# Kernel tuning notes

Measured on AMD Instinct MI355X. Metric: run time of the kernel, lower is better.

## Reference

```python
import jax, jax.numpy as jnp
import numpy as np

B, S = 512, 256          # batch, seq_len
C, H = 8, 16             # num_cells, expert hidden size
M = 20                   # memory_size (hard-coded in module)
NT = C * H               # num_trajectories = 128
ENC_IN = M * (NT + 1)    # 20*129 = 2580, memory_encode input dim
A_H = 16                 # agent LSTM hidden


def setup_inputs() -> dict:
    key = jax.random.key(0)
    ks = jax.random.split(key, 20)
    r = lambda i, shape: 0.1 * jax.random.normal(ks[i], shape, dtype=jnp.float32)
    return {
        "x": jax.random.normal(ks[0], (B, S, 1), dtype=jnp.float32),
        "pred0": jax.random.uniform(ks[1], (B, 1), dtype=jnp.float32),
        "gate0": jax.nn.softmax(jax.random.uniform(ks[2], (B, C), dtype=jnp.float32), axis=1),
        # experts: C parallel LSTM cells (input 1, hidden H) + per-cell scalar head
        "W_ih": r(3, (C, 4 * H, 1)), "W_hh": r(4, (C, 4 * H, H)),
        "b_ih": r(5, (C, 4 * H)), "b_hh": r(6, (C, 4 * H)),
        "W_o": r(7, (C, H)), "b_o": r(8, (C,)),
        # memory_encode: Linear(2580,64) ReLU Linear(64,16) ReLU
        "W1": r(9, (64, ENC_IN)), "b1": r(10, (64,)),
        "W2": r(11, (16, 64)), "b2": r(12, (16,)),
        # gate_linear: Linear(16, C) + softmax
        "Wg": r(13, (C, 16)), "bg": r(14, (C,)),
        # agent: 2 stacked LSTM cells (16 -> 16)
        "Wa_ih": r(15, (2, 4 * A_H, A_H)), "Wa_hh": r(16, (2, 4 * A_H, A_H)),
        "ba_ih": r(17, (2, 4 * A_H)), "ba_hh": r(18, (2, 4 * A_H)),
    }


def _cell(z, c):
    # PyTorch LSTMCell gate order: i, f, g, o
    i, f, g, o = jnp.split(z, 4, axis=-1)
    c2 = jax.nn.sigmoid(f) * c + jax.nn.sigmoid(i) * jnp.tanh(g)
    return jax.nn.sigmoid(o) * jnp.tanh(c2), c2


def reference(x, pred0, gate0, W_ih, W_hh, b_ih, b_hh, W_o, b_o,
              W1, b1, W2, b2, Wg, bg, Wa_ih, Wa_hh, ba_ih, ba_hh):
    mem0 = jnp.zeros((B, M, NT + 1), jnp.float32).at[:, :, -1].set(0.5)
    eh0 = jnp.zeros((B, H), jnp.float32)   # combined expert h (shared across cells)
    a0 = jnp.zeros((2, B, A_H), jnp.float32)

    def step(carry, x_t):
        mem, eh, ec, pred, gate_state, ah, ac = carry
        error = x_t - pred                                        # [B,1]
        # experts: C LSTM cells, all reading the shared combined state
        z = (jnp.einsum('bf,cgf->bcg', x_t, W_ih)
             + jnp.einsum('bh,cgh->bcg', eh, W_hh)
             + b_ih + b_hh)                                       # [B,C,4H]
        nh, nc = _cell(z, ec[:, None, :])                          # [B,C,H]
        o = jnp.einsum('bch,ch->bc', nh, W_o) + b_o               # [B,C]
        # memory_step: matmul(mstep, mem) shifts rows down by 1, row 0 <- w
        w = jnp.concatenate([nh.reshape(B, -1), error], axis=1)   # [B,NT+1]
        mem = jnp.concatenate([w[:, None, :], mem[:, :-1, :]], axis=1)
        # memory_encode MLP
        e1 = jax.nn.relu(mem.reshape(B, -1) @ W1.T + b1)
        ai = jax.nn.relu(e1 @ W2.T + b2)                           # [B,16]
        # agent: 2 stacked LSTM cells
        ah_l, ac_l, inp_l = [], [], ai
        for l in range(2):
            zl = inp_l @ Wa_ih[l].T + ba_ih[l] + ah[l] @ Wa_hh[l].T + ba_hh[l]
            hl, cl = _cell(zl, ac[l])
            ah_l.append(hl); ac_l.append(cl)
            inp_l = hl
        ah2, ac2 = jnp.stack(ah_l), jnp.stack(ac_l)
        gate = jax.nn.softmax(inp_l @ Wg.T + bg, axis=1)           # [B,C]
        # theta = clip(2.5 * mean|mem[:, :10, -1]|, 0, 1)  (relu(t)-relu(t-1))
        theta = jnp.clip(jnp.mean(jnp.abs(mem[:, :10, -1]), axis=1) * 2.5, 0.0, 1.0)[:, None]
        gate = gate * theta + gate_state * (1.0 - theta)
        eh2 = jnp.einsum('bc,bch->bh', gate, nh)                   # bmm(gate, h)
        ec2 = jnp.einsum('bc,bch->bh', gate, nc)
        pred2 = jnp.einsum('bc,bc->b', gate, o)[:, None]           # [B,1]
        return (mem, eh2, ec2, pred2, gate, ah2, ac2), pred2

    xs = jnp.swapaxes(x, 0, 1)  # [S,B,1]
    _, preds = jax.lax.scan(step, (mem0, eh0, eh0, pred0, gate0, a0, a0), xs)
    return jnp.swapaxes(preds, 0, 1)  # [B,S,1]
```

## Files before the change

kernel.cpp:

```cpp
#include <hip/hip_runtime.h>
#include <math.h>

#define S_LEN 256
#define NCELL 8
#define HID 16
#define MEM 20
#define NB 4
#define NTHR 512
#define RSTR 2592
#define RP 80

typedef _Float16 v8h __attribute__((ext_vector_type(8)));
typedef _Float16 v4h __attribute__((ext_vector_type(4)));
typedef float v4f __attribute__((ext_vector_type(4)));

__device__ __forceinline__ float sigm(float v) { return 1.0f / (1.0f + __expf(-v)); }
__device__ __forceinline__ float tanh_f(float v) { return 1.0f - 2.0f / (__expf(2.0f * v) + 1.0f); }
__device__ __forceinline__ float dot4(float4 a, float4 b) {
    return fmaf(a.x, b.x, fmaf(a.y, b.y, fmaf(a.z, b.z, a.w * b.w)));
}
__device__ __forceinline__ v4f mfma16(v8h a, v8h b, v4f c) {
    return __builtin_amdgcn_mfma_f32_16x16x32_f16(a, b, c, 0, 0, 0);
}

#define RING(b, s, k) ringH[(b) * RSTR + (s) * 128 + (k)]

__global__ __launch_bounds__(256)
void prep_w(const float* __restrict__ W1, const float* __restrict__ W_hh,
            const float* __restrict__ W_ih, const float* __restrict__ b_ih,
            const float* __restrict__ b_hh, _Float16* __restrict__ W1F,
            _Float16* __restrict__ WAF) {
    int idx = blockIdx.x * 256 + threadIdx.x;
    if (idx < 163840) {
        int e = idx & 7, lane = (idx >> 3) & 63, jt = (idx >> 9) & 3, t = idx >> 11;
        int m = t >> 2, kc = t & 3;
        int j = jt * 16 + (lane & 15);
        int k = kc * 32 + (lane >> 4) * 8 + e;
        W1F[idx] = (_Float16)W1[j * 2580 + m * 129 + k];
    } else if (idx < 163840 + 16384) {
        int d = idx - 163840;
        int e = d & 7, lane = (d >> 3) & 63, gate = (d >> 9) & 3, c = d >> 11;
        int m = lane & 15, k = (lane >> 4) * 8 + e;
        int row = c * 64 + gate * 16 + m;
        float v = 0.f;
        if (k < 16) v = W_hh[row * 16 + k];
        else if (k == 16) v = W_ih[row];
        else if (k == 17) v = b_ih[row] + b_hh[row];
        WAF[d] = (_Float16)v;
    }
}

#define E1P(BB, V) { \
    V = b1_l[lane] \
      + red[par][1][BB][lane] + red[par][2][BB][lane] + red[par][3][BB][lane] \
      + red[par][4][BB][lane] + red[par][5][BB][lane] + red[par][6][BB][lane] \
      + red[par][7][BB][lane]; }

#define E1F(BB, V) { \
    V += errdotS[BB][lane] \
       + red0[0][BB][lane] + red0[1][BB][lane] + red0[2][BB][lane] + red0[3][BB][lane]; \
    e1S[BB][lane] = fmaxf(V, 0.f); }

__global__ __attribute__((amdgpu_flat_work_group_size(NTHR, NTHR)))
void mmoe_kernel(const float* __restrict__ x, const float* __restrict__ pred0,
                 const float* __restrict__ gate0,
                 const float* __restrict__ W_ih, const float* __restrict__ W_hh,
                 const float* __restrict__ b_ih, const float* __restrict__ b_hh,
                 const float* __restrict__ W_o, const float* __restrict__ b_o,
                 const float* __restrict__ W1, const float* __restrict__ b1,
                 const float* __restrict__ W2, const float* __restrict__ b2,
                 const float* __restrict__ Wg, const float* __restrict__ bg,
                 const float* __restrict__ Wa_ih, const float* __restrict__ Wa_hh,
                 const float* __restrict__ ba_ih, const float* __restrict__ ba_hh,
                 const _Float16* __restrict__ W1F, const _Float16* __restrict__ WAF,
                 float* __restrict__ out)
{
    __shared__ __align__(16) _Float16 ringH[NB * RSTR];
    __shared__ __align__(16) _Float16 ehH[NB][40];
    __shared__ float errS[NB][MEM];
    __shared__ __align__(16) float WaI[2][64 * 20], WaH[2][64 * 20];
    __shared__ float ba_l[2][64];
    __shared__ __align__(16) float W2_l[16 * 68];
    __shared__ float b2_l[16];
    __shared__ __align__(16) float Wg_l[8][16], Wo_l[8][16];
    __shared__ float bg_l[8], bo_l[8];
    __shared__ float Werr_l[MEM * 64];
    __shared__ float b1_l[64];
    __shared__ float xS[NB][S_LEN];
    __shared__ __align__(16) float ecS[NB][HID];
    __shared__ __align__(16) float nhS[NCELL][NB][HID];
    __shared__ __align__(16) float ncS[NCELL][NB][HID];
    __shared__ float oS[NB][NCELL], predS[NB], gateS[NB][NCELL];
    __shared__ __align__(16) float ahS[2][NB][HID], acS[2][NB][HID];
    __shared__ __align__(16) float e1S[NB][64], aiS[NB][HID];
    __shared__ __align__(16) float glog[NB][8];
    __shared__ __align__(16) float red[2][8][NB][RP];
    __shared__ __align__(16) float red0[4][NB][RP];
    __shared__ float errdotS[NB][64];
    __shared__ float thS[NB];

    const int tid = threadIdx.x;
    const int b0 = blockIdx.x * NB;
    const int lane = tid & 63, wv = tid >> 6;
    const int quad = lane >> 4, nn = lane & 15, bb4 = nn & 3;

    for (int i = tid; i < 2048; i += NTHR) {
        int l = i >> 10, r = i & 1023, g = r >> 4, q = r & 15;
        WaI[l][g * 20 + q] = Wa_ih[i]; WaH[l][g * 20 + q] = Wa_hh[i];
    }
    for (int i = tid; i < 128; i += NTHR) { int l = i >> 6, g = i & 63; ba_l[l][g] = ba_ih[i] + ba_hh[i]; }
    for (int i = tid; i < 1024; i += NTHR) { int r = i >> 6, q = i & 63; W2_l[r * 68 + q] = W2[i]; }
    for (int i = tid; i < 1280; i += NTHR) { int m = i >> 6, j = i & 63; Werr_l[i] = W1[j * 2580 + m * 129 + 128]; }
    if (tid < 64) b1_l[tid] = b1[tid];
    if (tid < 16) b2_l[tid] = b2[tid];
    if (tid < 128) { int c = tid >> 4, h = tid & 15; Wg_l[c][h] = Wg[tid]; Wo_l[c][h] = W_o[tid]; }
    if (tid < 8) { bg_l[tid] = bg[tid]; bo_l[tid] = b_o[tid]; }
    for (int i = tid; i < NB * S_LEN; i += NTHR) { int b = i >> 8, s = i & 255; xS[b][s] = x[(b0 + b) * S_LEN + s]; }
    for (int i = tid; i < NB * RSTR; i += NTHR) ringH[i] = (_Float16)0.0f;
    for (int i = tid; i < 2 * 8 * NB * RP; i += NTHR) ((float*)red)[i] = 0.0f;
    if (tid < NB * 40) {
        int n = tid / 40, k = tid % 40;
        float v = 0.f;
        if (k == 16) v = x[(b0 + n) * S_LEN + 0];
        else if (k == 17) v = 1.0f;
        ehH[n][k] = (_Float16)v;
    }
    if (tid < NB * MEM) { int b = tid / MEM, m = tid % MEM; errS[b][m] = 0.5f; }
    if (tid < NB * HID) {
        int b = tid >> 4, h = tid & 15;
        ecS[b][h] = 0.f;
        ahS[0][b][h] = 0.f; ahS[1][b][h] = 0.f;
        acS[0][b][h] = 0.f; acS[1][b][h] = 0.f;
    }
    if (tid < NB) predS[tid] = pred0[b0 + tid];
    if (tid < NB * NCELL) { int b = tid >> 3, c = tid & 7; gateS[b][c] = gate0[(b0 + b) * NCELL + c]; }

    const v8h* WA = (const v8h*)WAF;
    v8h aI = WA[(wv * 4 + 0) * 64 + lane];
    v8h aF = WA[(wv * 4 + 1) * 64 + lane];
    v8h aG = WA[(wv * 4 + 2) * 64 + lane];
    v8h aO = WA[(wv * 4 + 3) * 64 + lane];
    const v8h* Wb = (const v8h*)W1F;
    const int kcW = wv >> 1, jt0W = (wv & 1) * 2;
    v8h m0A = Wb[(size_t)(kcW * 4 + jt0W) * 64 + lane];
    v8h m0B = Wb[(size_t)(kcW * 4 + jt0W + 1) * 64 + lane];
    __syncthreads();

    int head = 0;
    #pragma unroll 1
    for (int t = 0; t < S_LEN; ++t) {
        head = (head == 0) ? (MEM - 1) : (head - 1);
        const int par = t & 1, np = par ^ 1;
        float v0, v1, v2, v3;

        {
            v8h bfrag = *(const v8h*)&ehH[bb4][quad * 8];
            v4f z4 = {0.f, 0.f, 0.f, 0.f};
            v4f zi = mfma16(aI, bfrag, z4);
            v4f zf = mfma16(aF, bfrag, z4);
            v4f zg = mfma16(aG, bfrag, z4);
            v4f zo = mfma16(aO, bfrag, z4);
            if (nn < 4) {
                int b = nn, c = wv;
                v4f hv4, cv4; v4h hr;
                #pragma unroll
                for (int r = 0; r < 4; ++r) {
                    int h = quad * 4 + r;
                    float cc = ecS[b][h];
                    float c2 = sigm(zf[r]) * cc + sigm(zi[r]) * tanh_f(zg[r]);
                    float hv = sigm(zo[r]) * tanh_f(c2);
                    hv4[r] = hv; cv4[r] = c2; hr[r] = (_Float16)hv;
                }
                *(v4f*)&nhS[c][b][quad * 4] = hv4;
                *(v4f*)&ncS[c][b][quad * 4] = cv4;
                *(v4h*)&RING(b, head, c * 16 + quad * 4) = hr;
            }
            if (tid < NB) errS[tid][head] = xS[tid][t] - predS[tid];
        }
        __syncthreads();

        {
            v8h bfrag = *(const v8h*)&RING(bb4, head, kcW * 32 + quad * 8);
            v4f z = {0.f, 0.f, 0.f, 0.f};
            v4f c0 = mfma16(m0A, bfrag, z);
            v4f c1 = mfma16(m0B, bfrag, z);
            if (nn < 4) {
                *(v4f*)&red0[kcW][nn][jt0W * 16 + quad * 4] = c0;
                *(v4f*)&red0[kcW][nn][(jt0W + 1) * 16 + quad * 4] = c1;
            }
            if (wv == 0) {
                E1P(0, v0) E1P(1, v1) E1P(2, v2) E1P(3, v3)
            } else if (wv == 1) {
                if (lane < 32) {
                    int bb = lane >> 3, c = lane & 7;
                    const float4* np_ = (const float4*)&nhS[c][bb][0];
                    const float4* wp = (const float4*)&Wo_l[c][0];
                    float s = bo_l[c];
                    #pragma unroll
                    for (int q4 = 0; q4 < 4; ++q4) s += dot4(np_[q4], wp[q4]);
                    oS[bb][c] = s;
                }
            } else if (wv == 2) {
                if (lane < NB) {
                    float th = 0.f;
                    #pragma unroll
                    for (int m = 0; m < 10; ++m) {
                        int sl = head + m; if (sl >= MEM) sl -= MEM;
                        th += fabsf(errS[lane][sl]);
                    }
                    th *= 0.25f;
                    thS[lane] = fminf(fmaxf(th, 0.f), 1.f);
                }
            } else if (wv >= 3 && wv < 7) {
                int bb = wv - 3;
                float s = 0.f;
                int sl = head;
                #pragma unroll
                for (int m = 0; m < MEM; ++m) {
                    s = fmaf(Werr_l[m * 64 + lane], errS[bb][sl], s);
                    ++sl; if (sl >= MEM) sl = 0;
                }
                errdotS[bb][lane] = s;
            }
        }
        __syncthreads();

        if (wv >= 1) {
            int kt = (wv - 1) * 11;
            int ktEnd = kt + 11; if (ktEnd > 76) ktEnd = 76;
            v4f c0 = {0.f,0.f,0.f,0.f}, c1 = {0.f,0.f,0.f,0.f};
            v4f c2 = {0.f,0.f,0.f,0.f}, c3 = {0.f,0.f,0.f,0.f};
            size_t tb = (size_t)(4 + kt) * 256 + lane;
            v8h pA0 = Wb[tb], pA1 = Wb[tb + 64], pA2 = Wb[tb + 128], pA3 = Wb[tb + 192];
            int m0 = 1 + (kt >> 2), kc0 = kt & 3;
            int s0 = head + m0 - 1; if (s0 >= MEM) s0 -= MEM;
            v8h pB = *(const v8h*)&RING(bb4, s0, kc0 * 32 + quad * 8);
            #pragma unroll 1
            for (; kt < ktEnd; ++kt) {
                v8h A0 = pA0, A1 = pA1, A2 = pA2, A3 = pA3, B = pB;
                int kn = kt + 1;
                if (kn < ktEnd) {
                    size_t tn = (size_t)(4 + kn) * 256 + lane;
                    pA0 = Wb[tn]; pA1 = Wb[tn + 64]; pA2 = Wb[tn + 128]; pA3 = Wb[tn + 192];
                    int mn = 1 + (kn >> 2), kcn = kn & 3;
                    int sn = head + mn - 1; if (sn >= MEM) sn -= MEM;
                    pB = *(const v8h*)&RING(bb4, sn, kcn * 32 + quad * 8);
                }
                c0 = mfma16(A0, B, c0);
                c1 = mfma16(A1, B, c1);
                c2 = mfma16(A2, B, c2);
                c3 = mfma16(A3, B, c3);
            }
            if (nn < 4) {
                *(v4f*)&red[np][wv][nn][ 0 + quad * 4] = c0;
                *(v4f*)&red[np][wv][nn][16 + quad * 4] = c1;
                *(v4f*)&red[np][wv][nn][32 + quad * 4] = c2;
                *(v4f*)&red[np][wv][nn][48 + quad * 4] = c3;
            }
        } else {
            E1F(0, v0) E1F(1, v1) E1F(2, v2) E1F(3, v3)
            const int j = lane;
            {
                int bb = j >> 4, i = j & 15;
                const float4* epq = (const float4*)&e1S[bb][0];
                float s = b2_l[i];
                #pragma unroll
                for (int q = 0; q < 16; ++q) s += dot4(*(const float4*)&W2_l[i * 68 + q * 4], epq[q]);
                aiS[bb][i] = fmaxf(s, 0.f);
            }
            #pragma unroll
            for (int l = 0; l < 2; ++l) {
                int bb = j >> 4, h = j & 15;
                const float4* ip = (l == 0) ? (const float4*)&aiS[bb][0]
                                            : (const float4*)&ahS[0][bb][0];
                const float4* hp = (const float4*)&ahS[l][bb][0];
                float4 i0 = ip[0], i1 = ip[1], i2 = ip[2], i3 = ip[3];
                float4 h0 = hp[0], h1 = hp[1], h2v = hp[2], h3 = hp[3];
                float zg[4];
                #pragma unroll
                for (int gi = 0; gi < 4; ++gi) {
                    int g = gi * 16 + h;
                    const float* wi = &WaI[l][g * 20];
                    const float* wh = &WaH[l][g * 20];
                    float z = ba_l[l][g];
                    z += dot4(i0, *(const float4*)&wi[0]) + dot4(i1, *(const float4*)&wi[4])
                       + dot4(i2, *(const float4*)&wi[8]) + dot4(i3, *(const float4*)&wi[12]);
                    z += dot4(h0, *(const float4*)&wh[0]) + dot4(h1, *(const float4*)&wh[4])
                       + dot4(h2v, *(const float4*)&wh[8]) + dot4(h3, *(const float4*)&wh[12]);
                    zg[gi] = z;
                }
                float c2 = sigm(zg[1]) * acS[l][bb][h] + sigm(zg[0]) * tanh_f(zg[2]);
                acS[l][bb][h] = c2;
                ahS[l][bb][h] = sigm(zg[3]) * tanh_f(c2);
            }
            if (j < 32) {
                int bb = j >> 3, c = j & 7;
                const float4* hp = (const float4*)&ahS[1][bb][0];
                const float4* wg = (const float4*)&Wg_l[c][0];
                float s = bg_l[c];
                #pragma unroll
                for (int q = 0; q < 4; ++q) s += dot4(wg[q], hp[q]);
                glog[bb][c] = s;
                float4 ga = *(const float4*)&glog[bb][0];
                float4 gb = *(const float4*)&glog[bb][4];
                float mx = fmaxf(fmaxf(fmaxf(ga.x, ga.y), fmaxf(ga.z, ga.w)),
                                 fmaxf(fmaxf(gb.x, gb.y), fmaxf(gb.z, gb.w)));
                float sum = __expf(ga.x - mx) + __expf(ga.y - mx) + __expf(ga.z - mx) + __expf(ga.w - mx)
                          + __expf(gb.x - mx) + __expf(gb.y - mx) + __expf(gb.z - mx) + __expf(gb.w - mx);
                float p = __expf(s - mx) / sum;
                float th = thS[bb];
                gateS[bb][c] = p * th + gateS[bb][c] * (1.f - th);
            }
            {
                int bb = j >> 4, h = j & 15;
                float se = 0.f, sc = 0.f;
                #pragma unroll
                for (int c = 0; c < 8; ++c) {
                    float g = gateS[bb][c];
                    se = fmaf(g, nhS[c][bb][h], se);
                    sc = fmaf(g, ncS[c][bb][h], sc);
                }
                ehH[bb][h] = (_Float16)se;
                ecS[bb][h] = sc;
            }
            if (j < NB) {
                float s = 0.f;
                #pragma unroll
                for (int c = 0; c < 8; ++c) s = fmaf(gateS[j][c], oS[j][c], s);
                predS[j] = s;
                out[(b0 + j) * S_LEN + t] = s;
                ehH[j][16] = (_Float16)((t + 1 < S_LEN) ? xS[j][t + 1] : 0.f);
            }
        }
        __syncthreads();
    }
}

extern "C" void kernel_launch(void* const* d_in, const int* in_sizes, int n_in,
                              void* d_out, int out_size, void* d_ws, size_t ws_size,
                              hipStream_t stream) {
    const float* xp    = (const float*)d_in[0];
    const float* pred0 = (const float*)d_in[1];
    const float* gate0 = (const float*)d_in[2];
    const float* W_ih  = (const float*)d_in[3];
    const float* W_hh  = (const float*)d_in[4];
    const float* b_ih  = (const float*)d_in[5];
    const float* b_hh  = (const float*)d_in[6];
    const float* W_o   = (const float*)d_in[7];
    const float* b_o   = (const float*)d_in[8];
    const float* W1    = (const float*)d_in[9];
    const float* b1    = (const float*)d_in[10];
    const float* W2    = (const float*)d_in[11];
    const float* b2    = (const float*)d_in[12];
    const float* Wg    = (const float*)d_in[13];
    const float* bg    = (const float*)d_in[14];
    const float* Wa_ih = (const float*)d_in[15];
    const float* Wa_hh = (const float*)d_in[16];
    const float* ba_ih = (const float*)d_in[17];
    const float* ba_hh = (const float*)d_in[18];
    _Float16* W1F = (_Float16*)d_ws;
    _Float16* WAF = W1F + 163840;

    prep_w<<<(163840 + 16384 + 255) / 256, 256, 0, stream>>>(
        W1, W_hh, W_ih, b_ih, b_hh, W1F, WAF);
    mmoe_kernel<<<512 / NB, NTHR, 0, stream>>>(
        xp, pred0, gate0, W_ih, W_hh, b_ih, b_hh, W_o, b_o,
        W1, b1, W2, b2, Wg, bg, Wa_ih, Wa_hh, ba_ih, ba_hh,
        W1F, WAF, (float*)d_out);
}
```

Measured before the change: 1.282 ms.

## Fold newest-slot encoder matmul and side computations into serial wave to drop a barrier

Removes one per-step __syncthreads phase. The newest-memory-slot W1 contribution, the error dot product, the expert output heads and theta were split across all waves; now they are computed by the single serial wave, which runs 16 MFMAs with W1 fragments staged in LDS. This cuts barrier cost on every recurrent step, but lengthens the critical-path wave and adds 16KB of LDS.

```diff
diff --git a/kernel.cpp b/kernel.cpp
--- a/kernel.cpp
+++ b/kernel.cpp
@@ -50,17 +50,6 @@
     }
 }
 
-#define E1P(BB, V) { \
-    V = b1_l[lane] \
-      + red[par][1][BB][lane] + red[par][2][BB][lane] + red[par][3][BB][lane] \
-      + red[par][4][BB][lane] + red[par][5][BB][lane] + red[par][6][BB][lane] \
-      + red[par][7][BB][lane]; }
-
-#define E1F(BB, V) { \
-    V += errdotS[BB][lane] \
-       + red0[0][BB][lane] + red0[1][BB][lane] + red0[2][BB][lane] + red0[3][BB][lane]; \
-    e1S[BB][lane] = fmaxf(V, 0.f); }
-
 __global__ __attribute__((amdgpu_flat_work_group_size(NTHR, NTHR)))
 void mmoe_kernel(const float* __restrict__ x, const float* __restrict__ pred0,
                  const float* __restrict__ gate0,
@@ -76,6 +65,7 @@
                  float* __restrict__ out)
 {
     __shared__ __align__(16) _Float16 ringH[NB * RSTR];
+    __shared__ __align__(16) _Float16 W10F_l[8192];
     __shared__ __align__(16) _Float16 ehH[NB][40];
     __shared__ float errS[NB][MEM];
     __shared__ __align__(16) float WaI[2][64 * 20], WaH[2][64 * 20];
@@ -95,9 +85,7 @@
     __shared__ __align__(16) float e1S[NB][64], aiS[NB][HID];
     __shared__ __align__(16) float glog[NB][8];
     __shared__ __align__(16) float red[2][8][NB][RP];
-    __shared__ __align__(16) float red0[4][NB][RP];
-    __shared__ float errdotS[NB][64];
-    __shared__ float thS[NB];
+    __shared__ __align__(16) float red0f[NB][RP];
 
     const int tid = threadIdx.x;
     const int b0 = blockIdx.x * NB;
@@ -111,6 +99,7 @@
     for (int i = tid; i < 128; i += NTHR) { int l = i >> 6, g = i & 63; ba_l[l][g] = ba_ih[i] + ba_hh[i]; }
     for (int i = tid; i < 1024; i += NTHR) { int r = i >> 6, q = i & 63; W2_l[r * 68 + q] = W2[i]; }
     for (int i = tid; i < 1280; i += NTHR) { int m = i >> 6, j = i & 63; Werr_l[i] = W1[j * 2580 + m * 129 + 128]; }
+    for (int i = tid; i < 8192; i += NTHR) W10F_l[i] = W1F[i];
     if (tid < 64) b1_l[tid] = b1[tid];
     if (tid < 16) b2_l[tid] = b2[tid];
     if (tid < 128) { int c = tid >> 4, h = tid & 15; Wg_l[c][h] = Wg[tid]; Wo_l[c][h] = W_o[tid]; }
@@ -141,9 +130,7 @@
     v8h aG = WA[(wv * 4 + 2) * 64 + lane];
     v8h aO = WA[(wv * 4 + 3) * 64 + lane];
     const v8h* Wb = (const v8h*)W1F;
-    const int kcW = wv >> 1, jt0W = (wv & 1) * 2;
-    v8h m0A = Wb[(size_t)(kcW * 4 + jt0W) * 64 + lane];
-    v8h m0B = Wb[(size_t)(kcW * 4 + jt0W + 1) * 64 + lane];
+    const v8h* WL = (const v8h*)W10F_l;
     __syncthreads();
 
     int head = 0;
@@ -151,7 +138,6 @@
     for (int t = 0; t < S_LEN; ++t) {
         head = (head == 0) ? (MEM - 1) : (head - 1);
         const int par = t & 1, np = par ^ 1;
-        float v0, v1, v2, v3;
 
         {
             v8h bfrag = *(const v8h*)&ehH[bb4][quad * 8];
@@ -176,52 +162,6 @@
                 *(v4h*)&RING(b, head, c * 16 + quad * 4) = hr;
             }
             if (tid < NB) errS[tid][head] = xS[tid][t] - predS[tid];
-        }
-        __syncthreads();
-
-        {
-            v8h bfrag = *(const v8h*)&RING(bb4, head, kcW * 32 + quad * 8);
-            v4f z = {0.f, 0.f, 0.f, 0.f};
-            v4f c0 = mfma16(m0A, bfrag, z);
-            v4f c1 = mfma16(m0B, bfrag, z);
-            if (nn < 4) {
-                *(v4f*)&red0[kcW][nn][jt0W * 16 + quad * 4] = c0;
-                *(v4f*)&red0[kcW][nn][(jt0W + 1) * 16 + quad * 4] = c1;
-            }
-            if (wv == 0) {
-                E1P(0, v0) E1P(1, v1) E1P(2, v2) E1P(3, v3)
-            } else if (wv == 1) {
-                if (lane < 32) {
-                    int bb = lane >> 3, c = lane & 7;
-                    const float4* np_ = (const float4*)&nhS[c][bb][0];
-                    const float4* wp = (const float4*)&Wo_l[c][0];
-                    float s = bo_l[c];
-                    #pragma unroll
-                    for (int q4 = 0; q4 < 4; ++q4) s += dot4(np_[q4], wp[q4]);
-                    oS[bb][c] = s;
-                }
-            } else if (wv == 2) {
-                if (lane < NB) {
-                    float th = 0.f;
-                    #pragma unroll
-                    for (int m = 0; m < 10; ++m) {
-                        int sl = head + m; if (sl >= MEM) sl -= MEM;
-                        th += fabsf(errS[lane][sl]);
-                    }
-                    th *= 0.25f;
-                    thS[lane] = fminf(fmaxf(th, 0.f), 1.f);
-                }
-            } else if (wv >= 3 && wv < 7) {
-                int bb = wv - 3;
-                float s = 0.f;
-                int sl = head;
-                #pragma unroll
-                for (int m = 0; m < MEM; ++m) {
-                    s = fmaf(Werr_l[m * 64 + lane], errS[bb][sl], s);
-                    ++sl; if (sl >= MEM) sl = 0;
-                }
-                errdotS[bb][lane] = s;
-            }
         }
         __syncthreads();
 
@@ -258,8 +198,57 @@
                 *(v4f*)&red[np][wv][nn][48 + quad * 4] = c3;
             }
         } else {
-            E1F(0, v0) E1F(1, v1) E1F(2, v2) E1F(3, v3)
+            v4f z = {0.f, 0.f, 0.f, 0.f};
+            v4f a0 = z, a1 = z, a2 = z, a3 = z;
+            #pragma unroll
+            for (int kc = 0; kc < 4; ++kc) {
+                v8h bf = *(const v8h*)&RING(bb4, head, kc * 32 + quad * 8);
+                a0 = mfma16(WL[(kc * 4 + 0) * 64 + lane], bf, a0);
+                a1 = mfma16(WL[(kc * 4 + 1) * 64 + lane], bf, a1);
+                a2 = mfma16(WL[(kc * 4 + 2) * 64 + lane], bf, a2);
+                a3 = mfma16(WL[(kc * 4 + 3) * 64 + lane], bf, a3);
+            }
+            float v0 = b1_l[lane], v1 = v0, v2 = v0, v3 = v0;
+            #pragma unroll
+            for (int g = 1; g < 8; ++g) {
+                v0 += red[par][g][0][lane];
+                v1 += red[par][g][1][lane];
+                v2 += red[par][g][2][lane];
+                v3 += red[par][g][3][lane];
+            }
+            float ed0 = 0.f, ed1 = 0.f, ed2 = 0.f, ed3 = 0.f;
+            {
+                int sl = head;
+                #pragma unroll
+                for (int m = 0; m < MEM; ++m) {
+                    float w = Werr_l[m * 64 + lane];
+                    ed0 = fmaf(w, errS[0][sl], ed0);
+                    ed1 = fmaf(w, errS[1][sl], ed1);
+                    ed2 = fmaf(w, errS[2][sl], ed2);
+                    ed3 = fmaf(w, errS[3][sl], ed3);
+                    ++sl; if (sl >= MEM) sl = 0;
+                }
+            }
+            if (nn < 4) {
+                *(v4f*)&red0f[nn][ 0 + quad * 4] = a0;
+                *(v4f*)&red0f[nn][16 + quad * 4] = a1;
+                *(v4f*)&red0f[nn][32 + quad * 4] = a2;
+                *(v4f*)&red0f[nn][48 + quad * 4] = a3;
+            }
+            e1S[0][lane] = fmaxf(v0 + ed0 + red0f[0][lane], 0.f);
+            e1S[1][lane] = fmaxf(v1 + ed1 + red0f[1][lane], 0.f);
+            e1S[2][lane] = fmaxf(v2 + ed2 + red0f[2][lane], 0.f);
+            e1S[3][lane] = fmaxf(v3 + ed3 + red0f[3][lane], 0.f);
             const int j = lane;
+            if (j < 32) {
+                int bb = j >> 3, c = j & 7;
+                const float4* np_ = (const float4*)&nhS[c][bb][0];
+                const float4* wp = (const float4*)&Wo_l[c][0];
+                float s = bo_l[c];
+                #pragma unroll
+                for (int q4 = 0; q4 < 4; ++q4) s += dot4(np_[q4], wp[q4]);
+                oS[bb][c] = s;
+            }
             {
                 int bb = j >> 4, i = j & 15;
                 const float4* epq = (const float4*)&e1S[bb][0];
@@ -282,12 +271,12 @@
                     int g = gi * 16 + h;
                     const float* wi = &WaI[l][g * 20];
                     const float* wh = &WaH[l][g * 20];
-                    float z = ba_l[l][g];
-                    z += dot4(i0, *(const float4*)&wi[0]) + dot4(i1, *(const float4*)&wi[4])
-                       + dot4(i2, *(const float4*)&wi[8]) + dot4(i3, *(const float4*)&wi[12]);
-                    z += dot4(h0, *(const float4*)&wh[0]) + dot4(h1, *(const float4*)&wh[4])
-                       + dot4(h2v, *(const float4*)&wh[8]) + dot4(h3, *(const float4*)&wh[12]);
-                    zg[gi] = z;
+                    float zz = ba_l[l][g];
+                    zz += dot4(i0, *(const float4*)&wi[0]) + dot4(i1, *(const float4*)&wi[4])
+                        + dot4(i2, *(const float4*)&wi[8]) + dot4(i3, *(const float4*)&wi[12]);
+                    zz += dot4(h0, *(const float4*)&wh[0]) + dot4(h1, *(const float4*)&wh[4])
+                        + dot4(h2v, *(const float4*)&wh[8]) + dot4(h3, *(const float4*)&wh[12]);
+                    zg[gi] = zz;
                 }
                 float c2 = sigm(zg[1]) * acS[l][bb][h] + sigm(zg[0]) * tanh_f(zg[2]);
                 acS[l][bb][h] = c2;
@@ -308,7 +297,14 @@
                 float sum = __expf(ga.x - mx) + __expf(ga.y - mx) + __expf(ga.z - mx) + __expf(ga.w - mx)
                           + __expf(gb.x - mx) + __expf(gb.y - mx) + __expf(gb.z - mx) + __expf(gb.w - mx);
                 float p = __expf(s - mx) / sum;
-                float th = thS[bb];
+                float th = 0.f;
+                #pragma unroll
+                for (int m = 0; m < 10; ++m) {
+                    int sl = head + m; if (sl >= MEM) sl -= MEM;
+                    th += fabsf(errS[bb][sl]);
+                }
+                th *= 0.25f;
+                th = fminf(fmaxf(th, 0.f), 1.f);
                 gateS[bb][c] = p * th + gateS[bb][c] * (1.f - th);
             }
             {
```

After: 1.322 ms. 1.03x slower.

## Move memory-encode second layer and agent LSTM matvecs onto fp16 MFMA

Applied to the files above, without the earlier changes.

Repacks W2 and the agent LSTM weights into fp16 MFMA fragment layout in the prep kernel, then computes the 64->16 encode layer and both stacked agent LSTM cells with 16x16x32 MFMA instructions. This replaces the per-lane fp32 dot-product loops on the serial per-step critical path. Agent inputs and hidden states are kept as concatenated fp16 vectors so each cell needs one MFMA per gate. The cost is reduced precision on these activations and weights, and extra shared-memory staging buffers.

```diff
diff --git a/kernel.cpp b/kernel.cpp
--- a/kernel.cpp
+++ b/kernel.cpp
@@ -28,8 +28,10 @@
 __global__ __launch_bounds__(256)
 void prep_w(const float* __restrict__ W1, const float* __restrict__ W_hh,
             const float* __restrict__ W_ih, const float* __restrict__ b_ih,
-            const float* __restrict__ b_hh, _Float16* __restrict__ W1F,
-            _Float16* __restrict__ WAF) {
+            const float* __restrict__ b_hh, const float* __restrict__ W2,
+            const float* __restrict__ Wa_ih, const float* __restrict__ Wa_hh,
+            _Float16* __restrict__ W1F, _Float16* __restrict__ WAF,
+            _Float16* __restrict__ W2F, _Float16* __restrict__ WAGF) {
     int idx = blockIdx.x * 256 + threadIdx.x;
     if (idx < 163840) {
         int e = idx & 7, lane = (idx >> 3) & 63, jt = (idx >> 9) & 3, t = idx >> 11;
@@ -47,6 +49,19 @@
         else if (k == 16) v = W_ih[row];
         else if (k == 17) v = b_ih[row] + b_hh[row];
         WAF[d] = (_Float16)v;
+    } else if (idx < 163840 + 16384 + 1024) {
+        int d = idx - 163840 - 16384;
+        int e = d & 7, lane = (d >> 3) & 63, kc = d >> 9;
+        int i = lane & 15, k = kc * 32 + (lane >> 4) * 8 + e;
+        W2F[d] = (_Float16)W2[i * 64 + k];
+    } else if (idx < 163840 + 16384 + 1024 + 4096) {
+        int d = idx - 163840 - 16384 - 1024;
+        int e = d & 7, lane = (d >> 3) & 63, jt = (d >> 9) & 3, l = d >> 11;
+        int g = jt * 16 + (lane & 15);
+        int k = (lane >> 4) * 8 + e;
+        float v = (k < 16) ? Wa_ih[(l * 64 + g) * 16 + k]
+                           : Wa_hh[(l * 64 + g) * 16 + (k - 16)];
+        WAGF[d] = (_Float16)v;
     }
 }
 
@@ -55,11 +70,6 @@
       + red[par][1][BB][lane] + red[par][2][BB][lane] + red[par][3][BB][lane] \
       + red[par][4][BB][lane] + red[par][5][BB][lane] + red[par][6][BB][lane] \
       + red[par][7][BB][lane]; }
-
-#define E1F(BB, V) { \
-    V += errdotS[BB][lane] \
-       + red0[0][BB][lane] + red0[1][BB][lane] + red0[2][BB][lane] + red0[3][BB][lane]; \
-    e1S[BB][lane] = fmaxf(V, 0.f); }
 
 __global__ __attribute__((amdgpu_flat_work_group_size(NTHR, NTHR)))
 void mmoe_kernel(const float* __restrict__ x, const float* __restrict__ pred0,
@@ -73,14 +83,18 @@
                  const float* __restrict__ Wa_ih, const float* __restrict__ Wa_hh,
                  const float* __restrict__ ba_ih, const float* __restrict__ ba_hh,
                  const _Float16* __restrict__ W1F, const _Float16* __restrict__ WAF,
+                 const _Float16* __restrict__ W2F, const _Float16* __restrict__ WAGF,
                  float* __restrict__ out)
 {
     __shared__ __align__(16) _Float16 ringH[NB * RSTR];
     __shared__ __align__(16) _Float16 ehH[NB][40];
+    __shared__ __align__(16) _Float16 W2F_l[2 * 512];
+    __shared__ __align__(16) _Float16 WaG_l[2 * 4 * 512];
+    __shared__ __align__(16) _Float16 e1B[NB][64];
+    __shared__ __align__(16) _Float16 agB0[NB][32];
+    __shared__ __align__(16) _Float16 agB1[NB][32];
     __shared__ float errS[NB][MEM];
-    __shared__ __align__(16) float WaI[2][64 * 20], WaH[2][64 * 20];
     __shared__ float ba_l[2][64];
-    __shared__ __align__(16) float W2_l[16 * 68];
     __shared__ float b2_l[16];
     __shared__ __align__(16) float Wg_l[8][16], Wo_l[8][16];
     __shared__ float bg_l[8], bo_l[8];
@@ -91,8 +105,8 @@
     __shared__ __align__(16) float nhS[NCELL][NB][HID];
     __shared__ __align__(16) float ncS[NCELL][NB][HID];
     __shared__ float oS[NB][NCELL], predS[NB], gateS[NB][NCELL];
-    __shared__ __align__(16) float ahS[2][NB][HID], acS[2][NB][HID];
-    __shared__ __align__(16) float e1S[NB][64], aiS[NB][HID];
+    __shared__ __align__(16) float acS[2][NB][HID];
+    __shared__ __align__(16) float ah1S[NB][HID];
     __shared__ __align__(16) float glog[NB][8];
     __shared__ __align__(16) float red[2][8][NB][RP];
     __shared__ __align__(16) float red0[4][NB][RP];
@@ -104,12 +118,9 @@
     const int lane = tid & 63, wv = tid >> 6;
     const int quad = lane >> 4, nn = lane & 15, bb4 = nn & 3;
 
-    for (int i = tid; i < 2048; i += NTHR) {
-        int l = i >> 10, r = i & 1023, g = r >> 4, q = r & 15;
-        WaI[l][g * 20 + q] = Wa_ih[i]; WaH[l][g * 20 + q] = Wa_hh[i];
-    }
     for (int i = tid; i < 128; i += NTHR) { int l = i >> 6, g = i & 63; ba_l[l][g] = ba_ih[i] + ba_hh[i]; }
-    for (int i = tid; i < 1024; i += NTHR) { int r = i >> 6, q = i & 63; W2_l[r * 68 + q] = W2[i]; }
+    for (int i = tid; i < 1024; i += NTHR) W2F_l[i] = W2F[i];
+    for (int i = tid; i < 4096; i += NTHR) WaG_l[i] = WAGF[i];
     for (int i = tid; i < 1280; i += NTHR) { int m = i >> 6, j = i & 63; Werr_l[i] = W1[j * 2580 + m * 129 + 128]; }
     if (tid < 64) b1_l[tid] = b1[tid];
     if (tid < 16) b2_l[tid] = b2[tid];
@@ -118,6 +129,7 @@
     for (int i = tid; i < NB * S_LEN; i += NTHR) { int b = i >> 8, s = i & 255; xS[b][s] = x[(b0 + b) * S_LEN + s]; }
     for (int i = tid; i < NB * RSTR; i += NTHR) ringH[i] = (_Float16)0.0f;
     for (int i = tid; i < 2 * 8 * NB * RP; i += NTHR) ((float*)red)[i] = 0.0f;
+    for (int i = tid; i < NB * 32; i += NTHR) { ((_Float16*)agB0)[i] = (_Float16)0.0f; ((_Float16*)agB1)[i] = (_Float16)0.0f; }
     if (tid < NB * 40) {
         int n = tid / 40, k = tid % 40;
         float v = 0.f;
@@ -129,8 +141,8 @@
     if (tid < NB * HID) {
         int b = tid >> 4, h = tid & 15;
         ecS[b][h] = 0.f;
-        ahS[0][b][h] = 0.f; ahS[1][b][h] = 0.f;
         acS[0][b][h] = 0.f; acS[1][b][h] = 0.f;
+        ah1S[b][h] = 0.f;
     }
     if (tid < NB) predS[tid] = pred0[b0 + tid];
     if (tid < NB * NCELL) { int b = tid >> 3, c = tid & 7; gateS[b][c] = gate0[(b0 + b) * NCELL + c]; }
@@ -144,7 +156,12 @@
     const int kcW = wv >> 1, jt0W = (wv & 1) * 2;
     v8h m0A = Wb[(size_t)(kcW * 4 + jt0W) * 64 + lane];
     v8h m0B = Wb[(size_t)(kcW * 4 + jt0W + 1) * 64 + lane];
+    const v8h* W2Fv = (const v8h*)W2F_l;
+    const v8h* WaGv = (const v8h*)WaG_l;
     __syncthreads();
+    v4f b2v;
+    #pragma unroll
+    for (int r = 0; r < 4; ++r) b2v[r] = b2_l[quad * 4 + r];
 
     int head = 0;
     #pragma unroll 1
@@ -258,44 +275,81 @@
                 *(v4f*)&red[np][wv][nn][48 + quad * 4] = c3;
             }
         } else {
-            E1F(0, v0) E1F(1, v1) E1F(2, v2) E1F(3, v3)
+            {
+                float r0 = fmaxf(v0 + errdotS[0][lane]
+                       + red0[0][0][lane] + red0[1][0][lane] + red0[2][0][lane] + red0[3][0][lane], 0.f);
+                float r1 = fmaxf(v1 + errdotS[1][lane]
+                       + red0[0][1][lane] + red0[1][1][lane] + red0[2][1][lane] + red0[3][1][lane], 0.f);
+                float r2 = fmaxf(v2 + errdotS[2][lane]
+                       + red0[0][2][lane] + red0[1][2][lane] + red0[2][2][lane] + red0[3][2][lane], 0.f);
+                float r3 = fmaxf(v3 + errdotS[3][lane]
+                       + red0[0][3][lane] + red0[1][3][lane] + red0[2][3][lane] + red0[3][3][lane], 0.f);
+                e1B[0][lane] = (_Float16)r0;
+                e1B[1][lane] = (_Float16)r1;
+                e1B[2][lane] = (_Float16)r2;
+                e1B[3][lane] = (_Float16)r3;
+            }
+            {
+                v8h bk0 = *(const v8h*)&e1B[bb4][quad * 8];
+                v8h bk1 = *(const v8h*)&e1B[bb4][32 + quad * 8];
+                v4f cai = mfma16(W2Fv[lane], bk0, b2v);
+                cai = mfma16(W2Fv[64 + lane], bk1, cai);
+                if (nn < 4) {
+                    v4h av;
+                    #pragma unroll
+                    for (int r = 0; r < 4; ++r) av[r] = (_Float16)fmaxf(cai[r], 0.f);
+                    *(v4h*)&agB0[nn][quad * 4] = av;
+                }
+            }
+            {
+                v8h bf = *(const v8h*)&agB0[bb4][quad * 8];
+                v4f z4 = {0.f, 0.f, 0.f, 0.f};
+                v4f zi = mfma16(WaGv[0 * 64 + lane], bf, z4);
+                v4f zf = mfma16(WaGv[1 * 64 + lane], bf, z4);
+                v4f zg = mfma16(WaGv[2 * 64 + lane], bf, z4);
+                v4f zo = mfma16(WaGv[3 * 64 + lane], bf, z4);
+                if (nn < 4) {
+                    v4h hr;
+                    #pragma unroll
+                    for (int r = 0; r < 4; ++r) {
+                        int g = quad * 4 + r;
+                        float zi_ = zi[r] + ba_l[0][g], zf_ = zf[r] + ba_l[0][16 + g];
+                        float zg_ = zg[r] + ba_l[0][32 + g], zo_ = zo[r] + ba_l[0][48 + g];
+                        float c2 = sigm(zf_) * acS[0][nn][g] + sigm(zi_) * tanh_f(zg_);
+                        acS[0][nn][g] = c2;
+                        hr[r] = (_Float16)(sigm(zo_) * tanh_f(c2));
+                    }
+                    *(v4h*)&agB1[nn][quad * 4] = hr;
+                    *(v4h*)&agB0[nn][16 + quad * 4] = hr;
+                }
+            }
+            {
+                v8h bf = *(const v8h*)&agB1[bb4][quad * 8];
+                v4f z4 = {0.f, 0.f, 0.f, 0.f};
+                v4f zi = mfma16(WaGv[4 * 64 + lane], bf, z4);
+                v4f zf = mfma16(WaGv[5 * 64 + lane], bf, z4);
+                v4f zg = mfma16(WaGv[6 * 64 + lane], bf, z4);
+                v4f zo = mfma16(WaGv[7 * 64 + lane], bf, z4);
+                if (nn < 4) {
+                    v4h hr; v4f hf;
+                    #pragma unroll
+                    for (int r = 0; r < 4; ++r) {
+                        int g = quad * 4 + r;
+                        float zi_ = zi[r] + ba_l[1][g], zf_ = zf[r] + ba_l[1][16 + g];
+                        float zg_ = zg[r] + ba_l[1][32 + g], zo_ = zo[r] + ba_l[1][48 + g];
+                        float c2 = sigm(zf_) * acS[1][nn][g] + sigm(zi_) * tanh_f(zg_);
+                        acS[1][nn][g] = c2;
+                        float hv = sigm(zo_) * tanh_f(c2);
+                        hf[r] = hv; hr[r] = (_Float16)hv;
+                    }
+                    *(v4f*)&ah1S[nn][quad * 4] = hf;
+                    *(v4h*)&agB1[nn][16 + quad * 4] = hr;
+                }
+            }
             const int j = lane;
-            {
-                int bb = j >> 4, i = j & 15;
-                const float4* epq = (const float4*)&e1S[bb][0];
-                float s = b2_l[i];
-                #pragma unroll
-                for (int q = 0; q < 16; ++q) s += dot4(*(const float4*)&W2_l[i * 68 + q * 4], epq[q]);
-                aiS[bb][i] = fmaxf(s, 0.f);
-            }
-            #pragma unroll
-            for (int l = 0; l < 2; ++l) {
-                int bb = j >> 4, h = j & 15;
-                const float4* ip = (l == 0) ? (const float4*)&aiS[bb][0]
-                                            : (const float4*)&ahS[0][bb][0];
-                const float4* hp = (const float4*)&ahS[l][bb][0];
-                float4 i0 = ip[0], i1 = ip[1], i2 = ip[2], i3 = ip[3];
-                float4 h0 = hp[0], h1 = hp[1], h2v = hp[2], h3 = hp[3];
-                float zg[4];
-                #pragma unroll
-                for (int gi = 0; gi < 4; ++gi) {
-                    int g = gi * 16 + h;
-                    const float* wi = &WaI[l][g * 20];
-                    const float* wh = &WaH[l][g * 20];
-                    float z = ba_l[l][g];
-                    z += dot4(i0, *(const float4*)&wi[0]) + dot4(i1, *(const float4*)&wi[4])
-                       + dot4(i2, *(const float4*)&wi[8]) + dot4(i3, *(const float4*)&wi[12]);
-                    z += dot4(h0, *(const float4*)&wh[0]) + dot4(h1, *(const float4*)&wh[4])
-                       + dot4(h2v, *(const float4*)&wh[8]) + dot4(h3, *(const float4*)&wh[12]);
-                    zg[gi] = z;
-                }
-                float c2 = sigm(zg[1]) * acS[l][bb][h] + sigm(zg[0]) * tanh_f(zg[2]);
-                acS[l][bb][h] = c2;
-                ahS[l][bb][h] = sigm(zg[3]) * tanh_f(c2);
-            }
             if (j < 32) {
                 int bb = j >> 3, c = j & 7;
-                const float4* hp = (const float4*)&ahS[1][bb][0];
+                const float4* hp = (const float4*)&ah1S[bb][0];
                 const float4* wg = (const float4*)&Wg_l[c][0];
                 float s = bg_l[c];
                 #pragma unroll
@@ -358,13 +412,15 @@
     const float* Wa_hh = (const float*)d_in[16];
     const float* ba_ih = (const float*)d_in[17];
     const float* ba_hh = (const float*)d_in[18];
-    _Float16* W1F = (_Float16*)d_ws;
-    _Float16* WAF = W1F + 163840;
-
-    prep_w<<<(163840 + 16384 + 255) / 256, 256, 0, stream>>>(
-        W1, W_hh, W_ih, b_ih, b_hh, W1F, WAF);
+    _Float16* W1F  = (_Float16*)d_ws;
+    _Float16* WAF  = W1F + 163840;
+    _Float16* W2F  = WAF + 16384;
+    _Float16* WAGF = W2F + 1024;
+
+    prep_w<<<(163840 + 16384 + 1024 + 4096 + 255) / 256, 256, 0, stream>>>(
+        W1, W_hh, W_ih, b_ih, b_hh, W2, Wa_ih, Wa_hh, W1F, WAF, W2F, WAGF);
     mmoe_kernel<<<512 / NB, NTHR, 0, stream>>>(
         xp, pred0, gate0, W_ih, W_hh, b_ih, b_hh, W_o, b_o,
         W1, b1, W2, b2, Wg, bg, Wa_ih, Wa_hh, ba_ih, ba_hh,
-        W1F, WAF, (float*)d_out);
+        W1F, WAF, W2F, WAGF, (float*)d_out);
 }
```

Measured after the change: 1.272 ms. No clear change (-0.8%).
